# Kernel tuning notes

Measured on AMD Instinct MI355X. Metric: run time of the kernel, lower is better.

Reference implementation:

```python
import jax, jax.numpy as jnp
import numpy as np

D = 2048
NH = 16
DH = D // NH          # 128
DC = D // 4           # 512  (KV latent)
DCQ = D // 2          # 1024 (Q latent)
B = 1
L = 2048
MAX_LEN = 4096


def precompute_rope(dh, max_len):
    inv_freq = 1.0 / (10000.0 ** (jnp.arange(0, dh, 2, dtype=jnp.float32) / dh))
    t = jnp.arange(max_len, dtype=jnp.float32)
    freqs = jnp.outer(t, inv_freq)                 # [max_len, dh/2]
    emb = jnp.concatenate([freqs, freqs], axis=-1) # [max_len, dh]
    return jnp.cos(emb), jnp.sin(emb)


def apply_rope(t, cos, sin):
    # t: [B, H, L, dh]; cos/sin: [L, dh]
    x1, x2 = jnp.split(t, 2, axis=-1)
    rot = jnp.concatenate([-x2, x1], axis=-1)
    return t * cos + rot * sin


def setup_inputs() -> dict:
    key = jax.random.key(0)
    ks = jax.random.split(key, 9)
    s = 0.02
    return {
        "x": jax.random.normal(ks[0], (B, L, D), dtype=jnp.float32),
        "W_DKV": jax.random.normal(ks[1], (D, DC), dtype=jnp.float32) * s,
        "W_UK": jax.random.normal(ks[2], (DC, NH * DH), dtype=jnp.float32) * s,
        "W_UV": jax.random.normal(ks[3], (DC, NH * DH), dtype=jnp.float32) * s,
        "W_DQ": jax.random.normal(ks[4], (D, DCQ), dtype=jnp.float32) * s,
        "W_UQ": jax.random.normal(ks[5], (DCQ, 2 * NH * DH), dtype=jnp.float32) * s,
        "W_lam": jax.random.normal(ks[6], (D, NH), dtype=jnp.float32) * s,
        "b_lam": jnp.zeros((NH,), dtype=jnp.float32),
        "W_out": jax.random.normal(ks[7], (D, D), dtype=jnp.float32) * s,
    }


def reference(x, W_DKV, W_UK, W_UV, W_DQ, W_UQ, W_lam, b_lam, W_out):
    Bx, Lx, Dx = x.shape
    cos, sin = precompute_rope(DH, MAX_LEN)
    cos, sin = cos[:Lx], sin[:Lx]

    # MLA KV compression: single K/V shared by the paired query heads
    c_kv = x @ W_DKV                                            # [B, L, dc]
    k = (c_kv @ W_UK).reshape(Bx, Lx, NH, DH).transpose(0, 2, 1, 3)   # [B, nh, L, dh]
    v = (c_kv @ W_UV).reshape(Bx, Lx, NH, DH).transpose(0, 2, 1, 3)   # [B, nh, L, dh]

    # Low-rank Q, doubled heads for differential attention
    c_q = x @ W_DQ                                              # [B, L, dcq]
    q = (c_q @ W_UQ).reshape(Bx, Lx, 2 * NH, DH).transpose(0, 2, 1, 3)  # [B, 2nh, L, dh]

    q = apply_rope(q, cos, sin)
    k = apply_rope(k, cos, sin)

    # Group paired heads (2i, 2i+1) share k/v head i -> avoid repeat_interleave
    qp = q.reshape(Bx, NH, 2, Lx, DH)                           # [B, nh, 2, L, dh]
    scale = 1.0 / jnp.sqrt(jnp.asarray(DH, dtype=x.dtype))
    scores = jnp.einsum('bhpqd,bhkd->bhpqk', qp, k) * scale     # [B, nh, 2, L, L]
    causal = jnp.tril(jnp.ones((Lx, Lx), dtype=bool))
    scores = jnp.where(causal, scores, jnp.asarray(-jnp.inf, dtype=scores.dtype))
    probs = jax.nn.softmax(scores, axis=-1)
    attn = jnp.einsum('bhpqk,bhkd->bhpqd', probs, v)            # [B, nh, 2, L, dh]
    attn1, attn2 = attn[:, :, 0], attn[:, :, 1]                 # [B, nh, L, dh]

    # Token-specific sigmoid lambda per head
    lam = jax.nn.sigmoid(x @ W_lam + b_lam)                     # [B, L, nh]
    lam = lam.transpose(0, 2, 1)[..., None]                     # [B, nh, L, 1]

    out = (attn1 - lam * attn2).transpose(0, 2, 1, 3).reshape(Bx, Lx, Dx)
    return out @ W_out
```

## Files before the change

### kernel.cpp

```cpp
#include <hip/hip_runtime.h>
#include <cstdint>
#include <cstddef>

typedef __bf16 bf16x8 __attribute__((ext_vector_type(8)));
typedef __bf16 bf16x4 __attribute__((ext_vector_type(4)));
typedef float f32x4 __attribute__((ext_vector_type(4)));


template <int BM, bool BF16OUT>
__device__ __forceinline__ void gemm_body(const __bf16* __restrict__ A,
                                          const __bf16* __restrict__ Bt,
                                          void* __restrict__ Cv,
                                          int N, int K, int bm, int bn,
                                          __bf16* As, __bf16* Bs) {
  const int tid = threadIdx.x;
  const int w = tid >> 6;
  const int lane = tid & 63;
  const int quad = lane >> 4;
  const int l16 = lane & 15;
  constexpr int WM = (BM == 128) ? 64 : 32;
  constexpr int MI = WM / 16;
  const int wm = (w & 1) * WM;
  const int wn = (w >> 1) * 64;
  const int srow = lane >> 2;
  const int sseg = (lane & 3) * 8;

  auto stage = [&](int k0, int buf) {
#pragma unroll
    for (int g = 0; g < BM / 64; ++g) {
      const int grp = w + g * 4;
      const __bf16* ga = A + (size_t)(bm + grp * 16 + srow) * K + k0 + sseg;
      __builtin_amdgcn_global_load_lds(
          (const __attribute__((address_space(1))) void*)ga,
          (__attribute__((address_space(3))) void*)&As[buf * (BM * 32) + grp * 512],
          16, 0, 0);
    }
#pragma unroll
    for (int g = 0; g < 2; ++g) {
      const int grp = w + g * 4;
      const __bf16* gb = Bt + (size_t)(bn + grp * 16 + srow) * K + k0 + sseg;
      __builtin_amdgcn_global_load_lds(
          (const __attribute__((address_space(1))) void*)gb,
          (__attribute__((address_space(3))) void*)&Bs[buf * 4096 + grp * 512],
          16, 0, 0);
    }
  };

  f32x4 acc[MI][4];
#pragma unroll
  for (int i = 0; i < MI; ++i)
#pragma unroll
    for (int j = 0; j < 4; ++j) acc[i][j] = (f32x4){0.f, 0.f, 0.f, 0.f};

  asm volatile("s_waitcnt vmcnt(0)" ::: "memory");
  stage(0, 0);

  const int NIT = K >> 5;
  for (int it = 0; it < NIT; ++it) {
    const int cur = it & 1;
    if (it + 1 < NIT) {
      stage((it + 1) << 5, cur ^ 1);
      if constexpr (BM == 64)
        asm volatile("s_waitcnt vmcnt(3)" ::: "memory");
      else
        asm volatile("s_waitcnt vmcnt(4)" ::: "memory");
    } else {
      asm volatile("s_waitcnt vmcnt(0)" ::: "memory");
    }
    __builtin_amdgcn_s_barrier();
    asm volatile("" ::: "memory");
    const __bf16* Ab = &As[cur * (BM * 32)];
    const __bf16* Bb = &Bs[cur * 4096];
    bf16x8 af[MI], bfr[4];
#pragma unroll
    for (int i = 0; i < MI; ++i)
      af[i] = *(const bf16x8*)&Ab[(wm + i * 16 + l16) * 32 + quad * 8];
#pragma unroll
    for (int j = 0; j < 4; ++j)
      bfr[j] = *(const bf16x8*)&Bb[(wn + j * 16 + l16) * 32 + quad * 8];
#pragma unroll
    for (int i = 0; i < MI; ++i)
#pragma unroll
      for (int j = 0; j < 4; ++j)
        acc[i][j] = __builtin_amdgcn_mfma_f32_16x16x32_bf16(af[i], bfr[j],
                                                            acc[i][j], 0, 0, 0);
    asm volatile("s_waitcnt lgkmcnt(0)" ::: "memory");
    __builtin_amdgcn_s_barrier();
    asm volatile("" ::: "memory");
  }
#pragma unroll
  for (int i = 0; i < MI; ++i)
#pragma unroll
    for (int j = 0; j < 4; ++j)
#pragma unroll
      for (int r = 0; r < 4; ++r) {
        const int row = bm + wm + i * 16 + quad * 4 + r;
        const int col = bn + wn + j * 16 + l16;
        if constexpr (BF16OUT)
          ((__bf16*)Cv)[(size_t)row * N + col] = (__bf16)acc[i][j][r];
        else
          ((float*)Cv)[(size_t)row * N + col] = acc[i][j][r];
      }
}

template <int BM, bool BF16OUT>
__global__ __launch_bounds__(256) void gemm_mfma(const __bf16* __restrict__ A,
                                                 const __bf16* __restrict__ Bt,
                                                 void* __restrict__ Cv,
                                                 int M, int N, int K) {
  __shared__ __bf16 As[2 * BM * 32];
  __shared__ __bf16 Bs[2 * 128 * 32];
  gemm_body<BM, BF16OUT>(A, Bt, Cv, N, K, blockIdx.y * BM, blockIdx.x * 128, As, Bs);
}

template <int BM>
__global__ __launch_bounds__(256) void gemm_fused3(
    const __bf16* A0, const __bf16* B0, __bf16* C0, int N0, int K0, int nx0,
    const __bf16* A1, const __bf16* B1, __bf16* C1, int N1, int K1, int nx1,
    const __bf16* A2, const __bf16* B2, __bf16* C2, int N2, int K2) {
  __shared__ __bf16 As[2 * BM * 32];
  __shared__ __bf16 Bs[2 * 128 * 32];
  const int bx = blockIdx.x;
  const __bf16 *A, *Bt;
  __bf16* C;
  int N, K, bxl;
  if (bx < nx0)            { A = A0; Bt = B0; C = C0; N = N0; K = K0; bxl = bx; }
  else if (bx < nx0 + nx1) { A = A1; Bt = B1; C = C1; N = N1; K = K1; bxl = bx - nx0; }
  else                     { A = A2; Bt = B2; C = C2; N = N2; K = K2; bxl = bx - nx0 - nx1; }
  gemm_body<BM, true>(A, Bt, (void*)C, N, K, blockIdx.y * BM, bxl * 128, As, Bs);
}

__global__ __launch_bounds__(256) void prep_all(
    const float* __restrict__ W_DKV, const float* __restrict__ W_DQ,
    const float* __restrict__ W_UK,  const float* __restrict__ W_UV,
    const float* __restrict__ W_UQ,  const float* __restrict__ W_out,
    const float* __restrict__ x,     const float* __restrict__ W_lam,
    __bf16* __restrict__ tDKV, __bf16* __restrict__ tDQ,
    __bf16* __restrict__ tUK,  __bf16* __restrict__ tUV,
    __bf16* __restrict__ tUQ,  __bf16* __restrict__ tOut,
    __bf16* __restrict__ x_bf, __bf16* __restrict__ WlT,
    float* __restrict__ cosT, float* __restrict__ sinT) {
  __shared__ float T[32][36];
  int t = blockIdx.x;
  const int tid = threadIdx.x;
  if (t < 13312) {
    const float* src; __bf16* dst; int K, N, kx, ny;
    if (t < 1024)      {            src = W_DKV; dst = tDKV; K = 2048; N = 512;  kx = t & 63; ny = t >> 6; }
    else if (t < 3072) { t -= 1024; src = W_DQ;  dst = tDQ;  K = 2048; N = 1024; kx = t & 63; ny = t >> 6; }
    else if (t < 4096) { t -= 3072; src = W_UK;  dst = tUK;  K = 512;  N = 2048; kx = t & 15; ny = t >> 4; }
    else if (t < 5120) { t -= 4096; src = W_UV;  dst = tUV;  K = 512;  N = 2048; kx = t & 15; ny = t >> 4; }
    else if (t < 9216) { t -= 5120; src = W_UQ;  dst = tUQ;  K = 1024; N = 4096; kx = t & 31; ny = t >> 5; }
    else               { t -= 9216; src = W_out; dst = tOut; K = 2048; N = 2048; kx = t & 63; ny = t >> 6; }
    const int k0 = kx * 32;
    const int n0 = ny * 32;
    const int r = tid >> 3;
    const int c = (tid & 7) * 4;
    *(float4*)&T[r][c] = *(const float4*)&src[(size_t)(k0 + r) * N + n0 + c];
    __syncthreads();
    bf16x4 o = {(__bf16)T[c + 0][r], (__bf16)T[c + 1][r],
                (__bf16)T[c + 2][r], (__bf16)T[c + 3][r]};
    *(bf16x4*)&dst[(size_t)(n0 + r) * K + k0 + c] = o;
    return;
  }
  t -= 13312;
  if (t < 4096) {
    const int i = t * 256 + tid;
    float4 v = *(const float4*)&x[(size_t)i * 4];
    bf16x4 o = {(__bf16)v.x, (__bf16)v.y, (__bf16)v.z, (__bf16)v.w};
    *(bf16x4*)&x_bf[(size_t)i * 4] = o;
    return;
  }
  t -= 4096;
  if (t < 1024) {
    const int l = t * 2 + (tid >> 7);
    const int d = tid & 127;
    const int j = d & 63;
    const float inv = exp2f(-(float)j * 0.2076205059304601f);
    const float ang = (float)l * inv;
    cosT[l * 128 + d] = cosf(ang);
    sinT[l * 128 + d] = sinf(ang);
    return;
  }
  t -= 1024;
  {
    const int i = t * 256 + tid;
    const int k = i >> 4, n = i & 15;
    WlT[(size_t)n * 2048 + k] = (__bf16)W_lam[i];
  }
}

__global__ __launch_bounds__(256) void ropek_transv(__bf16* __restrict__ k_bf,
                                                    const float* __restrict__ cosT,
                                                    const float* __restrict__ sinT,
                                                    const __bf16* __restrict__ v_bf,
                                                    __bf16* __restrict__ v_t) {
  __shared__ float row[2048];
  __shared__ __align__(16) __bf16 Ts[32][40];
  int t = blockIdx.x;
  const int tid = threadIdx.x;
  if (t < 2048) {
    __bf16* rp = k_bf + (size_t)t * 2048;
#pragma unroll
    for (int i = 0; i < 2; ++i) {
      const int e4 = (tid + 256 * i) * 4;
      bf16x4 v = *(const bf16x4*)&rp[e4];
#pragma unroll
      for (int k = 0; k < 4; ++k) row[e4 + k] = (float)v[k];
    }
    __syncthreads();
#pragma unroll
    for (int i = 0; i < 8; ++i) {
      const int e = tid + 256 * i;
      const int d = e & 127;
      const float c = cosT[t * 128 + d];
      const float s = sinT[t * 128 + d];
      const float tv = row[e];
      const int base = e & ~127;
      const float rot = (d < 64) ? -row[base + d + 64] : row[base + d - 64];
      rp[e] = (__bf16)(tv * c + rot * s);
    }
    return;
  }
  t -= 2048;
  const int l0 = (t & 63) * 32;
  const int d0 = (t >> 6) * 32;
  const int r = tid >> 3;
  const int c = (tid & 7) * 4;
  *(bf16x4*)&Ts[r][c] = *(const bf16x4*)&v_bf[(size_t)(l0 + r) * 2048 + d0 + c];
  __syncthreads();
  bf16x4 o = {Ts[c + 0][r], Ts[c + 1][r], Ts[c + 2][r], Ts[c + 3][r]};
  *(bf16x4*)&v_t[(size_t)(d0 + r) * 2048 + l0 + c] = o;
}

__global__ __launch_bounds__(256) void lam_mfma_kernel(const __bf16* __restrict__ x_bf,
                                                       const __bf16* __restrict__ WlT,
                                                       const float* __restrict__ b_lam,
                                                       float* __restrict__ lam) {
  const int tid = threadIdx.x;
  const int w = tid >> 6, lane = tid & 63, quad = lane >> 4, l16 = lane & 15;
  const int m0 = (blockIdx.x * 4 + w) * 16;
  const __bf16* xrow = x_bf + (size_t)(m0 + l16) * 2048 + quad * 8;
  const __bf16* wrow = WlT + (size_t)l16 * 2048 + quad * 8;
  f32x4 acc[4];
#pragma unroll
  for (int u = 0; u < 4; ++u) acc[u] = (f32x4){0.f, 0.f, 0.f, 0.f};
  for (int k0 = 0; k0 < 2048; k0 += 128) {
#pragma unroll
    for (int u = 0; u < 4; ++u) {
      bf16x8 a = *(const bf16x8*)&xrow[k0 + u * 32];
      bf16x8 b = *(const bf16x8*)&wrow[k0 + u * 32];
      acc[u] = __builtin_amdgcn_mfma_f32_16x16x32_bf16(a, b, acc[u], 0, 0, 0);
    }
  }
  const float bl = b_lam[l16];
#pragma unroll
  for (int r = 0; r < 4; ++r) {
    const float v = acc[0][r] + acc[1][r] + acc[2][r] + acc[3][r] + bl;
    lam[(size_t)(m0 + quad * 4 + r) * 16 + l16] = 1.0f / (1.0f + __expf(-v));
  }
}

__global__ __launch_bounds__(256, 2) void attn_kernel3(
    const __bf16* __restrict__ Qb, const __bf16* __restrict__ Kb,
    const __bf16* __restrict__ Vt, const float* __restrict__ cosT,
    const float* __restrict__ sinT, const float* __restrict__ lam,
    __bf16* __restrict__ y) {
  __shared__ __align__(16) char smem[81920];
  float (*Ex)[132] = (float(*)[132])smem;

  const int bx = blockIdx.x;
  const int hv = bx >> 8;
  const int ii = bx & 255;
  const int qt = hv ? (ii >> 4) : 31 - (ii >> 4);
  const int hk = ii & 15;
  const int q0 = qt * 64;
  const int tid = threadIdx.x;
  const int w = tid >> 6, lane = tid & 63, quad = lane >> 4, l16 = lane & 15;
  const int wrow = (w & 1) * 32;
  const int qoff = (2 * hk + (w >> 1)) * 128;
  const int kvoff = hk * 128;
  const float qscale = 0.08838834764831845f;
  char* Pw = smem + 65536 + w * (32 * 128);

  bf16x8 aq[2][4];
#pragma unroll
  for (int s = 0; s < 2; ++s) {
    const int l = q0 + wrow + s * 16 + l16;
    const size_t qbase = (size_t)l * 4096 + qoff + quad * 8;
    bf16x8 raw[4];
#pragma unroll
    for (int ks = 0; ks < 4; ++ks)
      raw[ks] = *(const bf16x8*)&Qb[qbase + ks * 32];
#pragma unroll
    for (int ks = 0; ks < 4; ++ks) {
      const float* cp = &cosT[l * 128 + ks * 32 + quad * 8];
      const float* sp = &sinT[l * 128 + ks * 32 + quad * 8];
#pragma unroll
      for (int j = 0; j < 8; ++j) {
        const float cv = cp[j];
        const float sv = sp[j];
        const float rot = (ks < 2) ? -(float)raw[ks + 2][j] : (float)raw[ks - 2][j];
        aq[s][ks][j] = (__bf16)(((float)raw[ks][j] * cv + rot * sv) * qscale);
      }
    }
  }

  auto stage = [&](int kt_, char* buf) {
    const int k0_ = kt_ * 64;
    __bf16* Ksb = (__bf16*)buf;
    __bf16* Vsb = (__bf16*)(buf + 16384);
#pragma unroll
    for (int d = 0; d < 4; ++d) {
      const int r0 = w * 16 + d * 4;
      const int row = r0 + (lane >> 4);
      const int ck = (lane & 15) ^ (row & 15);
      const __bf16* ga = Kb + (size_t)(k0_ + row) * 2048 + kvoff + ck * 8;
      __builtin_amdgcn_global_load_lds(
          (const __attribute__((address_space(1))) void*)ga,
          (__attribute__((address_space(3))) void*)&Ksb[r0 * 128], 16, 0, 0);
      const int r0v = w * 32 + d * 8;
      const int rowv = r0v + (lane >> 3);
      const int cv = (lane & 7) ^ (rowv & 7);
      const __bf16* gv = Vt + (size_t)(kvoff + rowv) * 2048 + k0_ + cv * 8;
      __builtin_amdgcn_global_load_lds(
          (const __attribute__((address_space(1))) void*)gv,
          (__attribute__((address_space(3))) void*)&Vsb[r0v * 64], 16, 0, 0);
    }
  };

  f32x4 o[2][8];
#pragma unroll
  for (int s = 0; s < 2; ++s)
#pragma unroll
    for (int i = 0; i < 8; ++i) o[s][i] = (f32x4){0.f, 0.f, 0.f, 0.f};
  float m[2] = {-1e30f, -1e30f}, lsum[2] = {0.f, 0.f};

  asm volatile("s_waitcnt vmcnt(0)" ::: "memory");
  stage(0, smem);

  for (int kt = 0; kt <= qt; ++kt) {
    const int cur = kt & 1;
    __bf16* Ks = (__bf16*)(smem + cur * 32768);
    __bf16* Vs = (__bf16*)(smem + cur * 32768 + 16384);
    const int k0 = kt * 64;
    if (kt < qt) {
      stage(kt + 1, smem + (cur ^ 1) * 32768);
      asm volatile("s_waitcnt vmcnt(8)" ::: "memory");
    } else {
      asm volatile("s_waitcnt vmcnt(0)" ::: "memory");
    }
    __builtin_amdgcn_s_barrier();
    asm volatile("" ::: "memory");
    f32x4 st[2][4];
#pragma unroll
    for (int s = 0; s < 2; ++s)
#pragma unroll
      for (int t = 0; t < 4; ++t) st[s][t] = (f32x4){0.f, 0.f, 0.f, 0.f};
    __builtin_amdgcn_s_setprio(1);
#pragma unroll
    for (int ks = 0; ks < 4; ++ks) {
#pragma unroll
      for (int t = 0; t < 4; ++t) {
        bf16x8 ak = *(bf16x8*)&Ks[(t * 16 + l16) * 128 + (((ks * 4 + quad) ^ l16) << 3)];
        st[0][t] = __builtin_amdgcn_mfma_f32_16x16x32_bf16(ak, aq[0][ks], st[0][t], 0, 0, 0);
        st[1][t] = __builtin_amdgcn_mfma_f32_16x16x32_bf16(ak, aq[1][ks], st[1][t], 0, 0, 0);
      }
    }
    __builtin_amdgcn_s_setprio(0);
    const bool masked = (kt == qt);
#pragma unroll
    for (int s = 0; s < 2; ++s) {
      const int q = q0 + wrow + s * 16 + l16;
      float rm = -1e30f;
      if (!masked) {
#pragma unroll
        for (int t = 0; t < 4; ++t)
#pragma unroll
          for (int r = 0; r < 4; ++r) rm = fmaxf(rm, st[s][t][r]);
      } else {
#pragma unroll
        for (int t = 0; t < 4; ++t)
#pragma unroll
          for (int r = 0; r < 4; ++r) {
            const int key = k0 + t * 16 + quad * 4 + r;
            if (key > q) st[s][t][r] = -1e30f;
            rm = fmaxf(rm, st[s][t][r]);
          }
      }
      rm = fmaxf(rm, __shfl_xor(rm, 16, 64));
      rm = fmaxf(rm, __shfl_xor(rm, 32, 64));
      const float mn = fmaxf(m[s], rm);
      const float alpha = __expf(m[s] - mn);
      float rs = 0.f;
#pragma unroll
      for (int t = 0; t < 4; ++t)
#pragma unroll
        for (int r = 0; r < 4; ++r) {
          st[s][t][r] = __expf(st[s][t][r] - mn);
          rs += st[s][t][r];
        }
      rs += __shfl_xor(rs, 16, 64);
      rs += __shfl_xor(rs, 32, 64);
      m[s] = mn;
      lsum[s] = lsum[s] * alpha + rs;
      const int prow = s * 16 + l16;
#pragma unroll
      for (int t = 0; t < 4; ++t) {
        bf16x4 pk = {(__bf16)st[s][t][0], (__bf16)st[s][t][1],
                     (__bf16)st[s][t][2], (__bf16)st[s][t][3]};
        const int wch = (t * 2 + (quad >> 1)) ^ (prow & 7);
        *(bf16x4*)(Pw + prow * 128 + wch * 16 + (quad & 1) * 8) = pk;
      }
#pragma unroll
      for (int r = 0; r < 4; ++r) {
        const float ar = __shfl(alpha, quad * 4 + r, 64);
#pragma unroll
        for (int nt = 0; nt < 8; ++nt) o[s][nt][r] *= ar;
      }
    }
    __builtin_amdgcn_s_setprio(1);
#pragma unroll
    for (int ks = 0; ks < 2; ++ks) {
      const int rch = ((ks * 4 + quad) ^ (l16 & 7)) << 4;
      bf16x8 pa0 = *(bf16x8*)(Pw + l16 * 128 + rch);
      bf16x8 pa1 = *(bf16x8*)(Pw + (16 + l16) * 128 + rch);
#pragma unroll
      for (int nt = 0; nt < 8; ++nt) {
        bf16x8 bv = *(bf16x8*)&Vs[(nt * 16 + l16) * 64 + (((ks * 4 + quad) ^ (l16 & 7)) << 3)];
        o[0][nt] = __builtin_amdgcn_mfma_f32_16x16x32_bf16(pa0, bv, o[0][nt], 0, 0, 0);
        o[1][nt] = __builtin_amdgcn_mfma_f32_16x16x32_bf16(pa1, bv, o[1][nt], 0, 0, 0);
      }
    }
    __builtin_amdgcn_s_setprio(0);
    asm volatile("s_waitcnt lgkmcnt(0)" ::: "memory");
    __builtin_amdgcn_s_barrier();
    asm volatile("" ::: "memory");
  }
  if (w >= 2) {
#pragma unroll
    for (int s = 0; s < 2; ++s) {
      const float linv = 1.0f / lsum[s];
#pragma unroll
      for (int r = 0; r < 4; ++r) {
        const float inv = __shfl(linv, quad * 4 + r, 64);
        const int rr = wrow + s * 16 + quad * 4 + r;
#pragma unroll
        for (int nt = 0; nt < 8; ++nt)
          Ex[rr][nt * 16 + l16] = o[s][nt][r] * inv;
      }
    }
  }
  __syncthreads();
  if (w < 2) {
#pragma unroll
    for (int s = 0; s < 2; ++s) {
      const float linv = 1.0f / lsum[s];
#pragma unroll
      for (int r = 0; r < 4; ++r) {
        const float inv = __shfl(linv, quad * 4 + r, 64);
        const int rr = wrow + s * 16 + quad * 4 + r;
        const int l = q0 + rr;
        const float lm = lam[l * 16 + hk];
        __bf16* dst = y + (size_t)l * 2048 + hk * 128;
#pragma unroll
        for (int nt = 0; nt < 8; ++nt) {
          const float v1 = o[s][nt][r] * inv;
          dst[nt * 16 + l16] = (__bf16)(v1 - lm * Ex[rr][nt * 16 + l16]);
        }
      }
    }
  }
}

extern "C" void kernel_launch(void* const* d_in, const int* in_sizes, int n_in,
                              void* d_out, int out_size, void* d_ws, size_t ws_size,
                              hipStream_t stream) {
  const float* x     = (const float*)d_in[0];
  const float* W_DKV = (const float*)d_in[1];
  const float* W_UK  = (const float*)d_in[2];
  const float* W_UV  = (const float*)d_in[3];
  const float* W_DQ  = (const float*)d_in[4];
  const float* W_UQ  = (const float*)d_in[5];
  const float* W_lam = (const float*)d_in[6];
  const float* b_lam = (const float*)d_in[7];
  const float* W_out = (const float*)d_in[8];
  float* out = (float*)d_out;

  char* ws = (char*)d_ws;
  #define MB(n) ((size_t)(n) << 20)
  __bf16* x_bf   = (__bf16*)(ws + MB(0));
  __bf16* Wt_DKV = (__bf16*)(ws + MB(8));
  __bf16* Wt_DQ  = (__bf16*)(ws + MB(10));
  __bf16* c_kv   = (__bf16*)(ws + MB(14));
  __bf16* c_q    = (__bf16*)(ws + MB(16));
  __bf16* Wt_UK  = (__bf16*)(ws + MB(20));
  __bf16* Wt_UV  = (__bf16*)(ws + MB(22));
  __bf16* Wt_UQ  = (__bf16*)(ws + MB(24));
  __bf16* k_bf   = (__bf16*)(ws + MB(32));
  __bf16* v_bf   = (__bf16*)(ws + MB(40));
  __bf16* y_bf   = (__bf16*)(ws + MB(40));
  __bf16* q_bf   = (__bf16*)(ws + MB(48));
  __bf16* v_t    = (__bf16*)(ws + MB(64));
  float*  lam    = (float*)(ws + MB(88));
  float*  cosT   = (float*)(ws + MB(89));
  float*  sinT   = (float*)(ws + MB(90));
  __bf16* WlT    = (__bf16*)(ws + MB(91));
  __bf16* Wt_out = (__bf16*)(ws + MB(92));

  prep_all<<<18560, 256, 0, stream>>>(W_DKV, W_DQ, W_UK, W_UV, W_UQ, W_out,
                                      x, W_lam,
                                      Wt_DKV, Wt_DQ, Wt_UK, Wt_UV, Wt_UQ, Wt_out,
                                      x_bf, WlT, cosT, sinT);
  gemm_fused3<64><<<dim3(12, 32), 256, 0, stream>>>(
      x_bf, Wt_DKV, c_kv, 512, 2048, 4,
      x_bf, Wt_DQ,  c_q, 1024, 2048, 8,
      x_bf, Wt_DQ,  c_q, 1024, 2048);
  lam_mfma_kernel<<<32, 256, 0, stream>>>(x_bf, WlT, b_lam, lam);
  gemm_fused3<128><<<dim3(64, 16), 256, 0, stream>>>(
      c_kv, Wt_UK, k_bf, 2048, 512, 16,
      c_kv, Wt_UV, v_bf, 2048, 512, 16,
      c_q,  Wt_UQ, q_bf, 4096, 1024);
  ropek_transv<<<6144, 256, 0, stream>>>(k_bf, cosT, sinT, v_bf, v_t);
  attn_kernel3<<<512, 256, 0, stream>>>(q_bf, k_bf, v_t, cosT, sinT, lam, y_bf);
  gemm_mfma<64, false><<<dim3(16, 32), 256, 0, stream>>>(y_bf, Wt_out, out, 2048, 2048, 2048);
}
```

Measured before the change: 324.0 us.

## Split long causal attention tiles across KV halves and deepen GEMM k-staging

```diff
diff --git a/kernel.cpp b/kernel.cpp
--- a/kernel.cpp
+++ b/kernel.cpp
@@ -7,7 +7,15 @@
 typedef float f32x4 __attribute__((ext_vector_type(4)));
 
 
-template <int BM, bool BF16OUT>
+template <int N> __device__ __forceinline__ void waitcnt_vm() {
+  if constexpr (N == 3)      asm volatile("s_waitcnt vmcnt(3)" ::: "memory");
+  else if constexpr (N == 4) asm volatile("s_waitcnt vmcnt(4)" ::: "memory");
+  else if constexpr (N == 6) asm volatile("s_waitcnt vmcnt(6)" ::: "memory");
+  else if constexpr (N == 8) asm volatile("s_waitcnt vmcnt(8)" ::: "memory");
+  else                       asm volatile("s_waitcnt vmcnt(0)" ::: "memory");
+}
+
+template <int BM, int NKS, bool BF16OUT>
 __device__ __forceinline__ void gemm_body(const __bf16* __restrict__ A,
                                           const __bf16* __restrict__ Bt,
                                           void* __restrict__ Cv,
@@ -20,6 +28,7 @@
   const int l16 = lane & 15;
   constexpr int WM = (BM == 128) ? 64 : 32;
   constexpr int MI = WM / 16;
+  constexpr int NL = NKS * (BM / 64 + 2);
   const int wm = (w & 1) * WM;
   const int wn = (w >> 1) * 64;
   const int srow = lane >> 2;
@@ -27,22 +36,25 @@
 
   auto stage = [&](int k0, int buf) {
 #pragma unroll
-    for (int g = 0; g < BM / 64; ++g) {
-      const int grp = w + g * 4;
-      const __bf16* ga = A + (size_t)(bm + grp * 16 + srow) * K + k0 + sseg;
-      __builtin_amdgcn_global_load_lds(
-          (const __attribute__((address_space(1))) void*)ga,
-          (__attribute__((address_space(3))) void*)&As[buf * (BM * 32) + grp * 512],
-          16, 0, 0);
-    }
-#pragma unroll
-    for (int g = 0; g < 2; ++g) {
-      const int grp = w + g * 4;
-      const __bf16* gb = Bt + (size_t)(bn + grp * 16 + srow) * K + k0 + sseg;
-      __builtin_amdgcn_global_load_lds(
-          (const __attribute__((address_space(1))) void*)gb,
-          (__attribute__((address_space(3))) void*)&Bs[buf * 4096 + grp * 512],
-          16, 0, 0);
+    for (int ks = 0; ks < NKS; ++ks) {
+#pragma unroll
+      for (int g = 0; g < BM / 64; ++g) {
+        const int grp = w + g * 4;
+        const __bf16* ga = A + (size_t)(bm + grp * 16 + srow) * K + k0 + ks * 32 + sseg;
+        __builtin_amdgcn_global_load_lds(
+            (const __attribute__((address_space(1))) void*)ga,
+            (__attribute__((address_space(3))) void*)&As[(buf * NKS + ks) * (BM * 32) + grp * 512],
+            16, 0, 0);
+      }
+#pragma unroll
+      for (int g = 0; g < 2; ++g) {
+        const int grp = w + g * 4;
+        const __bf16* gb = Bt + (size_t)(bn + grp * 16 + srow) * K + k0 + ks * 32 + sseg;
+        __builtin_amdgcn_global_load_lds(
+            (const __attribute__((address_space(1))) void*)gb,
+            (__attribute__((address_space(3))) void*)&Bs[(buf * NKS + ks) * 4096 + grp * 512],
+            16, 0, 0);
+      }
     }
   };
 
@@ -55,35 +67,35 @@
   asm volatile("s_waitcnt vmcnt(0)" ::: "memory");
   stage(0, 0);
 
-  const int NIT = K >> 5;
+  const int NIT = K / (32 * NKS);
   for (int it = 0; it < NIT; ++it) {
     const int cur = it & 1;
     if (it + 1 < NIT) {
-      stage((it + 1) << 5, cur ^ 1);
-      if constexpr (BM == 64)
-        asm volatile("s_waitcnt vmcnt(3)" ::: "memory");
-      else
-        asm volatile("s_waitcnt vmcnt(4)" ::: "memory");
+      stage((it + 1) * 32 * NKS, cur ^ 1);
+      waitcnt_vm<NL>();
     } else {
-      asm volatile("s_waitcnt vmcnt(0)" ::: "memory");
+      waitcnt_vm<0>();
     }
     __builtin_amdgcn_s_barrier();
     asm volatile("" ::: "memory");
-    const __bf16* Ab = &As[cur * (BM * 32)];
-    const __bf16* Bb = &Bs[cur * 4096];
-    bf16x8 af[MI], bfr[4];
-#pragma unroll
-    for (int i = 0; i < MI; ++i)
-      af[i] = *(const bf16x8*)&Ab[(wm + i * 16 + l16) * 32 + quad * 8];
-#pragma unroll
-    for (int j = 0; j < 4; ++j)
-      bfr[j] = *(const bf16x8*)&Bb[(wn + j * 16 + l16) * 32 + quad * 8];
-#pragma unroll
-    for (int i = 0; i < MI; ++i)
+    const __bf16* Ab = &As[cur * NKS * (BM * 32)];
+    const __bf16* Bb = &Bs[cur * NKS * 4096];
+#pragma unroll
+    for (int ks = 0; ks < NKS; ++ks) {
+      bf16x8 af[MI], bfr[4];
+#pragma unroll
+      for (int i = 0; i < MI; ++i)
+        af[i] = *(const bf16x8*)&Ab[ks * (BM * 32) + (wm + i * 16 + l16) * 32 + quad * 8];
 #pragma unroll
       for (int j = 0; j < 4; ++j)
-        acc[i][j] = __builtin_amdgcn_mfma_f32_16x16x32_bf16(af[i], bfr[j],
-                                                            acc[i][j], 0, 0, 0);
+        bfr[j] = *(const bf16x8*)&Bb[ks * 4096 + (wn + j * 16 + l16) * 32 + quad * 8];
+#pragma unroll
+      for (int i = 0; i < MI; ++i)
+#pragma unroll
+        for (int j = 0; j < 4; ++j)
+          acc[i][j] = __builtin_amdgcn_mfma_f32_16x16x32_bf16(af[i], bfr[j],
+                                                              acc[i][j], 0, 0, 0);
+    }
     asm volatile("s_waitcnt lgkmcnt(0)" ::: "memory");
     __builtin_amdgcn_s_barrier();
     asm volatile("" ::: "memory");
@@ -103,23 +115,23 @@
       }
 }
 
-template <int BM, bool BF16OUT>
+template <int BM, int NKS, bool BF16OUT>
 __global__ __launch_bounds__(256) void gemm_mfma(const __bf16* __restrict__ A,
                                                  const __bf16* __restrict__ Bt,
                                                  void* __restrict__ Cv,
                                                  int M, int N, int K) {
-  __shared__ __bf16 As[2 * BM * 32];
-  __shared__ __bf16 Bs[2 * 128 * 32];
-  gemm_body<BM, BF16OUT>(A, Bt, Cv, N, K, blockIdx.y * BM, blockIdx.x * 128, As, Bs);
-}
-
-template <int BM>
+  __shared__ __bf16 As[2 * 128 * 32 * NKS > 2 * BM * 32 * NKS ? 2 * BM * 32 * NKS : 2 * BM * 32 * NKS];
+  __shared__ __bf16 Bs[2 * 128 * 32 * NKS];
+  gemm_body<BM, NKS, BF16OUT>(A, Bt, Cv, N, K, blockIdx.y * BM, blockIdx.x * 128, As, Bs);
+}
+
+template <int BM, int NKS>
 __global__ __launch_bounds__(256) void gemm_fused3(
     const __bf16* A0, const __bf16* B0, __bf16* C0, int N0, int K0, int nx0,
     const __bf16* A1, const __bf16* B1, __bf16* C1, int N1, int K1, int nx1,
     const __bf16* A2, const __bf16* B2, __bf16* C2, int N2, int K2) {
-  __shared__ __bf16 As[2 * BM * 32];
-  __shared__ __bf16 Bs[2 * 128 * 32];
+  __shared__ __bf16 As[2 * BM * 32 * NKS];
+  __shared__ __bf16 Bs[2 * 128 * 32 * NKS];
   const int bx = blockIdx.x;
   const __bf16 *A, *Bt;
   __bf16* C;
@@ -127,7 +139,7 @@
   if (bx < nx0)            { A = A0; Bt = B0; C = C0; N = N0; K = K0; bxl = bx; }
   else if (bx < nx0 + nx1) { A = A1; Bt = B1; C = C1; N = N1; K = K1; bxl = bx - nx0; }
   else                     { A = A2; Bt = B2; C = C2; N = N2; K = K2; bxl = bx - nx0 - nx1; }
-  gemm_body<BM, true>(A, Bt, (void*)C, N, K, blockIdx.y * BM, bxl * 128, As, Bs);
+  gemm_body<BM, NKS, true>(A, Bt, (void*)C, N, K, blockIdx.y * BM, bxl * 128, As, Bs);
 }
 
 __global__ __launch_bounds__(256) void prep_all(
@@ -260,20 +272,33 @@
   }
 }
 
+__device__ const unsigned char SQT[48] = {
+    31, 31, 30, 15,  30, 29, 29, 28, 14,  28, 27, 27, 26, 13,
+    26, 25, 25, 24, 12,  24, 23, 23, 22, 11,  22, 21, 21, 20, 10,
+    20, 19, 19, 18, 9,  18, 17, 17, 16, 8,  16, 7,  6, 5, 4, 3, 2, 1, 0};
+__device__ const unsigned char SH[48] = {
+    1, 2, 1, 0,  2, 1, 2, 1, 0,  2, 1, 2, 1, 0,
+    2, 1, 2, 1, 0,  2, 1, 2, 1, 0,  2, 1, 2, 1, 0,
+    2, 1, 2, 1, 0,  2, 1, 2, 1, 0,  2, 0,  0, 0, 0, 0, 0, 0, 0};
+
 __global__ __launch_bounds__(256, 2) void attn_kernel3(
     const __bf16* __restrict__ Qb, const __bf16* __restrict__ Kb,
     const __bf16* __restrict__ Vt, const float* __restrict__ cosT,
     const float* __restrict__ sinT, const float* __restrict__ lam,
-    __bf16* __restrict__ y) {
+    __bf16* __restrict__ y, float* __restrict__ Opart,
+    float* __restrict__ Mlp) {
   __shared__ __align__(16) char smem[81920];
   float (*Ex)[132] = (float(*)[132])smem;
 
   const int bx = blockIdx.x;
-  const int hv = bx >> 8;
-  const int ii = bx & 255;
-  const int qt = hv ? (ii >> 4) : 31 - (ii >> 4);
-  const int hk = ii & 15;
+  const int slot = bx >> 4;
+  const int hk = bx & 15;
+  const int qt = SQT[slot];
+  const int hf = SH[slot];
   const int q0 = qt * 64;
+  const int half = (qt + 2) >> 1;
+  const int kt_lo = (hf == 2) ? half : 0;
+  const int kt_hi = (hf == 1) ? half : qt + 1;
   const int tid = threadIdx.x;
   const int w = tid >> 6, lane = tid & 63, quad = lane >> 4, l16 = lane & 15;
   const int wrow = (w & 1) * 32;
@@ -336,14 +361,14 @@
   float m[2] = {-1e30f, -1e30f}, lsum[2] = {0.f, 0.f};
 
   asm volatile("s_waitcnt vmcnt(0)" ::: "memory");
-  stage(0, smem);
-
-  for (int kt = 0; kt <= qt; ++kt) {
-    const int cur = kt & 1;
+  stage(kt_lo, smem);
+
+  for (int kt = kt_lo; kt < kt_hi; ++kt) {
+    const int cur = (kt - kt_lo) & 1;
     __bf16* Ks = (__bf16*)(smem + cur * 32768);
     __bf16* Vs = (__bf16*)(smem + cur * 32768 + 16384);
     const int k0 = kt * 64;
-    if (kt < qt) {
+    if (kt + 1 < kt_hi) {
       stage(kt + 1, smem + (cur ^ 1) * 32768);
       asm volatile("s_waitcnt vmcnt(8)" ::: "memory");
     } else {
@@ -436,39 +461,89 @@
     __builtin_amdgcn_s_barrier();
     asm volatile("" ::: "memory");
   }
-  if (w >= 2) {
+  if (hf == 0) {
+    if (w >= 2) {
+#pragma unroll
+      for (int s = 0; s < 2; ++s) {
+        const float linv = 1.0f / lsum[s];
+#pragma unroll
+        for (int r = 0; r < 4; ++r) {
+          const float inv = __shfl(linv, quad * 4 + r, 64);
+          const int rr = wrow + s * 16 + quad * 4 + r;
+#pragma unroll
+          for (int nt = 0; nt < 8; ++nt)
+            Ex[rr][nt * 16 + l16] = o[s][nt][r] * inv;
+        }
+      }
+    }
+    __syncthreads();
+    if (w < 2) {
+#pragma unroll
+      for (int s = 0; s < 2; ++s) {
+        const float linv = 1.0f / lsum[s];
+#pragma unroll
+        for (int r = 0; r < 4; ++r) {
+          const float inv = __shfl(linv, quad * 4 + r, 64);
+          const int rr = wrow + s * 16 + quad * 4 + r;
+          const int l = q0 + rr;
+          const float lm = lam[l * 16 + hk];
+          __bf16* dst = y + (size_t)l * 2048 + hk * 128;
+#pragma unroll
+          for (int nt = 0; nt < 8; ++nt) {
+            const float v1 = o[s][nt][r] * inv;
+            dst[nt * 16 + l16] = (__bf16)(v1 - lm * Ex[rr][nt * 16 + l16]);
+          }
+        }
+      }
+    }
+  } else {
+    const int ti = (((qt - 16) * 16 + hk) * 2 + (w >> 1)) * 2 + (hf - 1);
+    float* Ob = Opart + (size_t)ti * 8192;
 #pragma unroll
     for (int s = 0; s < 2; ++s) {
-      const float linv = 1.0f / lsum[s];
+      if (lane < 16)
+        *(float2*)&Mlp[(size_t)ti * 128 + (wrow + s * 16 + l16) * 2] =
+            (float2){m[s], lsum[s]};
 #pragma unroll
       for (int r = 0; r < 4; ++r) {
-        const float inv = __shfl(linv, quad * 4 + r, 64);
         const int rr = wrow + s * 16 + quad * 4 + r;
 #pragma unroll
         for (int nt = 0; nt < 8; ++nt)
-          Ex[rr][nt * 16 + l16] = o[s][nt][r] * inv;
-      }
-    }
-  }
-  __syncthreads();
-  if (w < 2) {
-#pragma unroll
-    for (int s = 0; s < 2; ++s) {
-      const float linv = 1.0f / lsum[s];
-#pragma unroll
-      for (int r = 0; r < 4; ++r) {
-        const float inv = __shfl(linv, quad * 4 + r, 64);
-        const int rr = wrow + s * 16 + quad * 4 + r;
-        const int l = q0 + rr;
-        const float lm = lam[l * 16 + hk];
-        __bf16* dst = y + (size_t)l * 2048 + hk * 128;
-#pragma unroll
-        for (int nt = 0; nt < 8; ++nt) {
-          const float v1 = o[s][nt][r] * inv;
-          dst[nt * 16 + l16] = (__bf16)(v1 - lm * Ex[rr][nt * 16 + l16]);
-        }
-      }
-    }
+          Ob[rr * 128 + nt * 16 + l16] = o[s][nt][r];
+      }
+    }
+  }
+}
+
+__global__ __launch_bounds__(256) void attn_combine(
+    const float* __restrict__ Op, const float* __restrict__ Ml,
+    const float* __restrict__ lam, __bf16* __restrict__ y) {
+  const int b = blockIdx.x;
+  const int qt16 = b >> 6;
+  const int hk = (b >> 2) & 15;
+  const int r0 = (b & 3) * 16;
+  const int tid = threadIdx.x;
+  const int d = tid & 127;
+  const int rbase = r0 + (tid >> 7);
+  const int tb = (qt16 * 16 + hk) * 4;
+#pragma unroll
+  for (int k = 0; k < 8; ++k) {
+    const int rr = rbase + k * 2;
+    const int l = (qt16 + 16) * 64 + rr;
+    float Oh[2];
+#pragma unroll
+    for (int h01 = 0; h01 < 2; ++h01) {
+      const int t1 = tb + h01 * 2, t2 = t1 + 1;
+      const float m1 = Ml[t1 * 128 + rr * 2], l1 = Ml[t1 * 128 + rr * 2 + 1];
+      const float m2 = Ml[t2 * 128 + rr * 2], l2 = Ml[t2 * 128 + rr * 2 + 1];
+      const float mm = fmaxf(m1, m2);
+      const float a1 = __expf(m1 - mm), a2 = __expf(m2 - mm);
+      const float inv = 1.0f / (l1 * a1 + l2 * a2);
+      Oh[h01] = (a1 * Op[(size_t)t1 * 8192 + rr * 128 + d] +
+                 a2 * Op[(size_t)t2 * 8192 + rr * 128 + d]) * inv;
+    }
+    const float lm = lam[(size_t)l * 16 + hk];
+    y[(size_t)l * 2048 + hk * 128 + d] = (__bf16)(Oh[0] - lm * Oh[1]);
   }
 }
 
@@ -506,21 +581,25 @@
   float*  sinT   = (float*)(ws + MB(90));
   __bf16* WlT    = (__bf16*)(ws + MB(91));
   __bf16* Wt_out = (__bf16*)(ws + MB(92));
+  float*  Opart  = (float*)(ws + MB(0));
+  float*  Mlp    = (float*)(ws + MB(88) + 131072);
 
   prep_all<<<18560, 256, 0, stream>>>(W_DKV, W_DQ, W_UK, W_UV, W_UQ, W_out,
                                       x, W_lam,
                                       Wt_DKV, Wt_DQ, Wt_UK, Wt_UV, Wt_UQ, Wt_out,
                                       x_bf, WlT, cosT, sinT);
-  gemm_fused3<64><<<dim3(12, 32), 256, 0, stream>>>(
+  gemm_fused3<64, 2><<<dim3(12, 32), 256, 0, stream>>>(
       x_bf, Wt_DKV, c_kv, 512, 2048, 4,
       x_bf, Wt_DQ,  c_q, 1024, 2048, 8,
       x_bf, Wt_DQ,  c_q, 1024, 2048);
   lam_mfma_kernel<<<32, 256, 0, stream>>>(x_bf, WlT, b_lam, lam);
-  gemm_fused3<128><<<dim3(64, 16), 256, 0, stream>>>(
+  gemm_fused3<128, 1><<<dim3(64, 16), 256, 0, stream>>>(
       c_kv, Wt_UK, k_bf, 2048, 512, 16,
       c_kv, Wt_UV, v_bf, 2048, 512, 16,
       c_q,  Wt_UQ, q_bf, 4096, 1024);
   ropek_transv<<<6144, 256, 0, stream>>>(k_bf, cosT, sinT, v_bf, v_t);
-  attn_kernel3<<<512, 256, 0, stream>>>(q_bf, k_bf, v_t, cosT, sinT, lam, y_bf);
-  gemm_mfma<64, false><<<dim3(16, 32), 256, 0, stream>>>(y_bf, Wt_out, out, 2048, 2048, 2048);
-}
+  attn_kernel3<<<768, 256, 0, stream>>>(q_bf, k_bf, v_t, cosT, sinT, lam, y_bf,
+                                        Opart, Mlp);
+  attn_combine<<<1024, 256, 0, stream>>>(Opart, Mlp, lam, y_bf);
+  gemm_mfma<64, 2, false><<<dim3(16, 32), 256, 0, stream>>>(y_bf, Wt_out, out, 2048, 2048, 2048);
+}
```

Result: no change. 328.0 us (+1.2%).
